# Performance work log

Measured on AMD Instinct MI355X. Metric: run time of the kernel, lower is better.

Reference implementation:

```python
import jax, jax.numpy as jnp
import numpy as np

T = 2048          # num tokens (single prefill sequence)
H = 32            # num local heads
HIDDEN = 5120
Q_LORA = 1536
KV_LORA = 512
D_NOPE = 128
D_ROPE = 64
D_QK = D_NOPE + D_ROPE   # 192
D_V = 128
EPS = 1e-6
SCALING = D_QK ** -0.5


def _rope_tables(theta=10000.0):
    inv_freq = 1.0 / (theta ** (np.arange(0, D_ROPE, 2, dtype=np.float32) / D_ROPE))
    t = np.arange(T, dtype=np.float32)
    freqs = np.outer(t, inv_freq)                       # [T, D_ROPE/2]
    emb = np.concatenate([freqs, freqs], axis=-1)       # [T, D_ROPE]
    return (jnp.asarray(np.cos(emb))[:, None, :],       # [T,1,D_ROPE]
            jnp.asarray(np.sin(emb))[:, None, :])


def setup_inputs() -> dict:
    key = jax.random.key(0)
    ks = jax.random.split(key, 6)
    cos, sin = _rope_tables()
    s = lambda fan_in: 1.0 / np.sqrt(fan_in)
    return {
        'hidden_states': jax.random.normal(ks[0], (T, HIDDEN), jnp.float32),
        'cos': cos,
        'sin': sin,
        'wq_a': jax.random.normal(ks[1], (HIDDEN, Q_LORA), jnp.float32) * s(HIDDEN),
        'q_a_ln_w': jnp.ones((Q_LORA,), jnp.float32),
        'wq_b': jax.random.normal(ks[2], (Q_LORA, H * D_QK), jnp.float32) * s(Q_LORA),
        'wkv_a': jax.random.normal(ks[3], (HIDDEN, KV_LORA + D_ROPE), jnp.float32) * s(HIDDEN),
        'kv_a_ln_w': jnp.ones((KV_LORA,), jnp.float32),
        'wkv_b': jax.random.normal(ks[4], (KV_LORA, H * (D_NOPE + D_V)), jnp.float32) * s(KV_LORA),
        'wo': jax.random.normal(ks[5], (H * D_V, HIDDEN), jnp.float32) * s(H * D_V),
    }


def _rmsnorm(x, w):
    var = jnp.mean(jnp.square(x), axis=-1, keepdims=True)
    return x * jax.lax.rsqrt(var + EPS) * w


def _deinterleave(x):
    # torch: x.view(..., d//2, 2).transpose(-1,-2).reshape(..., d)
    return jnp.concatenate([x[..., 0::2], x[..., 1::2]], axis=-1)


def _rotate_half(x):
    h = x.shape[-1] // 2
    return jnp.concatenate([-x[..., h:], x[..., :h]], axis=-1)


def _apply_rope(q, k, cos, sin):
    q = _deinterleave(q)
    k = _deinterleave(k)
    return q * cos + _rotate_half(q) * sin, k * cos + _rotate_half(k) * sin


def reference(hidden_states, cos, sin, wq_a, q_a_ln_w, wq_b, wkv_a, kv_a_ln_w, wkv_b, wo):
    # Q path: low-rank down-proj, RMSNorm, up-proj
    q = _rmsnorm(hidden_states @ wq_a, q_a_ln_w) @ wq_b
    q = q.reshape(T, H, D_QK)
    q_nope, q_pe = q[..., :D_NOPE], q[..., D_NOPE:]

    # KV path: joint compressed latent + rope key slice
    ckv = hidden_states @ wkv_a
    compressed, k_pe = ckv[..., :KV_LORA], ckv[..., KV_LORA:].reshape(T, 1, D_ROPE)
    kv = (_rmsnorm(compressed, kv_a_ln_w) @ wkv_b).reshape(T, H, D_NOPE + D_V)
    k_nope, value = kv[..., :D_NOPE], kv[..., D_NOPE:]

    # split RoPE on the rope sub-dims only
    q_pe, k_pe = _apply_rope(q_pe, k_pe, cos, sin)
    q = jnp.concatenate([q_nope, q_pe], axis=-1)                    # [T,H,192]
    k = jnp.concatenate([k_nope, jnp.broadcast_to(k_pe, (T, H, D_ROPE))], axis=-1)

    # causal attention (prefill)
    scores = jnp.einsum('qhd,khd->hqk', q, k) * SCALING             # [H,T,T]
    mask = jnp.tril(jnp.ones((T, T), bool))
    scores = jnp.where(mask[None], scores, jnp.finfo(scores.dtype).min)
    probs = jax.nn.softmax(scores, axis=-1)
    attn = jnp.einsum('hqk,khd->qhd', probs, value)                 # [T,H,128]

    return attn.reshape(T, H * D_V) @ wo                            # [T,HIDDEN]
```

## Files before the change

kernel.cpp:

```cpp
#include <hip/hip_runtime.h>
#include <hip/hip_bf16.h>
#include <stdint.h>

typedef __hip_bfloat16 bf16;
typedef short v8s __attribute__((ext_vector_type(8)));
typedef float v4f __attribute__((ext_vector_type(4)));

#define T_SEQ 2048
#define NH 32
#define HIDDEN_D 5120
#define QL 1536
#define KVL 512
#define DQK 192
#define DV 128
#define NAB 2176
#define SCALE_QK 0.07216878364870322f

static __device__ __forceinline__ float b2f(bf16 x) { return __bfloat162float(x); }
static __device__ __forceinline__ bf16 f2b(float x) { return __float2bfloat16(x); }
static __device__ __forceinline__ unsigned short bbits(bf16 x) {
  union { bf16 b; unsigned short u; } c; c.b = x; return c.u;
}

#define AS1(p) ((__attribute__((address_space(1))) void*)(p))
#define AS3(p) ((__attribute__((address_space(3))) void*)(p))

__global__ void detect_k(const void* __restrict__ lnw, int* __restrict__ flag) {
  if (threadIdx.x == 0 && blockIdx.x == 0) {
    uint32_t u = *(const uint32_t*)lnw;
    flag[0] = ((u & 0xFFFFu) == 0x3F80u) ? 1 : 0;
  }
}

__global__ __launch_bounds__(256) void conv_bf16(const void* __restrict__ in,
        bf16* __restrict__ out, const int* __restrict__ flag, int n4) {
  int i = blockIdx.x * 256 + threadIdx.x;
  if (i >= n4) return;
  if (flag[0]) {
    ((uint2*)out)[i] = ((const uint2*)in)[i];
  } else {
    float4 v = ((const float4*)in)[i];
    uint2 o;
    o.x = ((uint32_t)bbits(f2b(v.y)) << 16) | bbits(f2b(v.x));
    o.y = ((uint32_t)bbits(f2b(v.w)) << 16) | bbits(f2b(v.z));
    ((uint2*)out)[i] = o;
  }
}

__global__ __launch_bounds__(256) void transpose_any(const void* __restrict__ in,
        bf16* __restrict__ out, int R, int C, int Cpad, const int* __restrict__ flag) {
  __shared__ unsigned short tile[32][33];
  const int isb = flag[0];
  int c0 = blockIdx.x * 32, r0 = blockIdx.y * 32;
  int tx = threadIdx.x, ty = threadIdx.y;
#pragma unroll
  for (int i = 0; i < 32; i += 8) {
    unsigned short v = 0;
    int c = c0 + tx;
    if (c < C) {
      size_t idx = (size_t)(r0 + ty + i) * C + c;
      v = isb ? *((const unsigned short*)in + idx)
              : bbits(f2b(((const float*)in)[idx]));
    }
    tile[ty + i][tx] = v;
  }
  __syncthreads();
#pragma unroll
  for (int i = 0; i < 32; i += 8) {
    int c = c0 + ty + i;
    if (c < Cpad) *(unsigned short*)&out[(size_t)c * R + r0 + tx] = tile[tx][ty + i];
  }
}

template <bool FINAL>
__global__ __launch_bounds__(256, 2)
void gemm_bt(const bf16* __restrict__ A, const bf16* __restrict__ Bt,
             void* __restrict__ C, const int* __restrict__ flag,
             int M, int N, int K) {
  __shared__ __align__(16) bf16 As[128 * 32];
  __shared__ __align__(16) bf16 Bs[128 * 32];
  const int tid = threadIdx.x;
  const int wv = tid >> 6;
  const int lane = tid & 63;
  const int quad = lane >> 4;
  const int c16 = lane & 15;
  const int wm = (wv & 1) * 64;
  const int wn = (wv >> 1) * 64;
  const int m0 = blockIdx.y * 128;
  const int n0 = blockIdx.x * 128;

  v4f acc[4][4] = {};

  const int r0 = tid >> 2;
  const int cc0 = (tid & 3) << 3;

  for (int k0 = 0; k0 < K; k0 += 32) {
    __syncthreads();
#pragma unroll
    for (int i = 0; i < 2; ++i) {
      int r = r0 + i * 64;
      const bf16* ga = A + (size_t)(m0 + r) * K + k0 + cc0;
      const bf16* gb = Bt + (size_t)(n0 + r) * K + k0 + cc0;
      __builtin_amdgcn_global_load_lds(AS1(ga), AS3(As + (i * 256 + wv * 64) * 8), 16, 0, 0);
      __builtin_amdgcn_global_load_lds(AS1(gb), AS3(Bs + (i * 256 + wv * 64) * 8), 16, 0, 0);
    }
    __syncthreads();
    v8s af[4], bfr[4];
#pragma unroll
    for (int t = 0; t < 4; ++t)
      af[t] = *(const v8s*)(As + (wm + t * 16 + c16) * 32 + quad * 8);
#pragma unroll
    for (int t = 0; t < 4; ++t)
      bfr[t] = *(const v8s*)(Bs + (wn + t * 16 + c16) * 32 + quad * 8);
#pragma unroll
    for (int i = 0; i < 4; ++i)
#pragma unroll
      for (int j = 0; j < 4; ++j)
        acc[i][j] = __builtin_amdgcn_mfma_f32_16x16x32_bf16(af[i], bfr[j], acc[i][j], 0, 0, 0);
  }
  const bool outBf = FINAL ? (flag[0] != 0) : true;
#pragma unroll
  for (int i = 0; i < 4; ++i)
#pragma unroll
    for (int j = 0; j < 4; ++j) {
      int m = m0 + wm + i * 16 + quad * 4;
      int n = n0 + wn + j * 16 + c16;
#pragma unroll
      for (int r = 0; r < 4; ++r) {
        if (outBf) ((bf16*)C)[(size_t)(m + r) * N + n] = f2b(acc[i][j][r]);
        else       ((float*)C)[(size_t)(m + r) * N + n] = acc[i][j][r];
      }
    }
}

template <int N>
__global__ __launch_bounds__(256) void rmsnorm_k(const bf16* __restrict__ in,
        const void* __restrict__ w, const int* __restrict__ flag,
        bf16* __restrict__ out, int strideIn, int strideOut) {
  constexpr int CNT = N / 256;
  const int row = blockIdx.x, tid = threadIdx.x;
  const int isb = flag[0];
  const bf16* x = in + (size_t)row * strideIn;
  float v[CNT];
  float ss = 0.f;
#pragma unroll
  for (int i = 0; i < CNT; ++i) { v[i] = b2f(x[tid + i * 256]); ss += v[i] * v[i]; }
#pragma unroll
  for (int o = 32; o > 0; o >>= 1) ss += __shfl_xor(ss, o);
  __shared__ float wsum[4];
  if ((tid & 63) == 0) wsum[tid >> 6] = ss;
  __syncthreads();
  float scale = rsqrtf((wsum[0] + wsum[1] + wsum[2] + wsum[3]) / (float)N + 1e-6f);
#pragma unroll
  for (int i = 0; i < CNT; ++i) {
    int c = tid + i * 256;
    float wv = isb ? b2f(((const bf16*)w)[c]) : ((const float*)w)[c];
    out[(size_t)row * strideOut + c] = f2b(v[i] * scale * wv);
  }
}

__global__ __launch_bounds__(256) void qk_build(const bf16* __restrict__ qraw,
        const bf16* __restrict__ ckv, const bf16* __restrict__ kv,
        const void* __restrict__ cosb, const void* __restrict__ sinb,
        const int* __restrict__ flag,
        bf16* __restrict__ Qh, bf16* __restrict__ Kh) {
  const int t = blockIdx.x, tid = threadIdx.x;
  const int isb = flag[0];
  __shared__ float cs[64], sn[64], kpe[64];
  if (tid < 64) {
    int j = tid;
    float c = isb ? b2f(((const bf16*)cosb)[t * 64 + j]) : ((const float*)cosb)[t * 64 + j];
    float s = isb ? b2f(((const bf16*)sinb)[t * 64 + j]) : ((const float*)sinb)[t * 64 + j];
    cs[j] = c; sn[j] = s;
    const bf16* kp = ckv + (size_t)t * NAB + 512;
    float v;
    if (j < 32) v = b2f(kp[2 * j]) * c - b2f(kp[2 * j + 1]) * s;
    else { int i2 = j - 32; v = b2f(kp[2 * i2 + 1]) * c + b2f(kp[2 * i2]) * s; }
    kpe[j] = v;
  }
  __syncthreads();
  for (int idx = tid; idx < 512; idx += 256) {
    int h = idx >> 4, d8 = (idx & 15) * 8;
    *(uint4*)&Qh[((size_t)h * T_SEQ + t) * DQK + d8] =
        *(const uint4*)&qraw[(size_t)t * 6144 + h * DQK + d8];
    *(uint4*)&Kh[((size_t)h * T_SEQ + t) * DQK + d8] =
        *(const uint4*)&kv[(size_t)t * 8192 + h * 256 + d8];
  }
  for (int idx = tid; idx < 2048; idx += 256) {
    int h = idx >> 6, j = idx & 63;
    const bf16* qp = qraw + (size_t)t * 6144 + h * DQK + 128;
    float v;
    if (j < 32) v = b2f(qp[2 * j]) * cs[j] - b2f(qp[2 * j + 1]) * sn[j];
    else { int i2 = j - 32; v = b2f(qp[2 * i2 + 1]) * cs[j] + b2f(qp[2 * i2]) * sn[j]; }
    Qh[((size_t)h * T_SEQ + t) * DQK + 128 + j] = f2b(v);
    Kh[((size_t)h * T_SEQ + t) * DQK + 128 + j] = f2b(kpe[j]);
  }
}

__global__ __launch_bounds__(256) void vt_build(const bf16* __restrict__ kv,
                                                bf16* __restrict__ VT) {
  __shared__ unsigned short tile[32][33];
  int h = blockIdx.z;
  int t0 = blockIdx.x * 32, d0 = blockIdx.y * 32;
  int tx = threadIdx.x, ty = threadIdx.y;
#pragma unroll
  for (int i = 0; i < 32; i += 8)
    tile[ty + i][tx] = *(const unsigned short*)
        &kv[(size_t)(t0 + ty + i) * 8192 + h * 256 + 128 + d0 + tx];
  __syncthreads();
#pragma unroll
  for (int i = 0; i < 32; i += 8)
    *(unsigned short*)&VT[((size_t)h * DV + d0 + ty + i) * T_SEQ + t0 + tx] = tile[tx][ty + i];
}

__global__ __launch_bounds__(256, 2)
void mla_attn(const bf16* __restrict__ Qh, const bf16* __restrict__ Kh,
              const bf16* __restrict__ VT, bf16* __restrict__ attn) {
  const int wg = blockIdx.x + blockIdx.y * 16;
  const int swz = (wg & 7) * 64 + (wg >> 3);
  const int pid = swz & 15, h = swz >> 4;
  const int tid = threadIdx.x, wv = tid >> 6, lane = tid & 63;
  const int quad = lane >> 4, c16 = lane & 15;

  __shared__ __align__(16) bf16 Ksh[64 * 200];
  __shared__ __align__(16) bf16 Vsh[128 * 72];
  __shared__ __align__(16) bf16 Psh[4 * 16 * 72];
  bf16* pw = Psh + wv * (16 * 72);

#pragma unroll 1
  for (int pass = 0; pass < 2; ++pass) {
    const int qt = (pass == 0) ? pid : (31 - pid);
    const int qbase = qt * 64;

    v8s qf[6];
    {
      const bf16* qp = Qh + ((size_t)h * T_SEQ + qbase + wv * 16 + c16) * DQK;
#pragma unroll
      for (int ks = 0; ks < 6; ++ks) qf[ks] = *(const v8s*)(qp + ks * 32 + quad * 8);
    }

    v4f oacc[8] = {};
    float mrow[4] = {-1e30f, -1e30f, -1e30f, -1e30f};
    float lrow[4] = {0.f, 0.f, 0.f, 0.f};

    for (int kt = 0; kt <= qt; ++kt) {
      const int kb = kt * 64;
      __syncthreads();
      for (int c = tid; c < 1536; c += 256) {
        int r = c / 24, off = (c % 24) * 8;
        *(uint4*)(Ksh + r * 200 + off) =
            *(const uint4*)(Kh + ((size_t)h * T_SEQ + kb + r) * DQK + off);
      }
      for (int c = tid; c < 1024; c += 256) {
        int r = c >> 3, off = (c & 7) * 8;
        *(uint4*)(Vsh + r * 72 + off) =
            *(const uint4*)(VT + ((size_t)h * DV + r) * T_SEQ + kb + off);
      }
      __syncthreads();

      v4f sacc[4] = {};
#pragma unroll
      for (int nt = 0; nt < 4; ++nt)
#pragma unroll
        for (int ks = 0; ks < 6; ++ks) {
          v8s kf = *(const v8s*)(Ksh + (nt * 16 + c16) * 200 + ks * 32 + quad * 8);
          sacc[nt] = __builtin_amdgcn_mfma_f32_16x16x32_bf16(qf[ks], kf, sacc[nt], 0, 0, 0);
        }

      float rmax[4] = {-1e30f, -1e30f, -1e30f, -1e30f};
      const int rowg = qbase + wv * 16 + quad * 4;
#pragma unroll
      for (int nt = 0; nt < 4; ++nt) {
        int col = kb + nt * 16 + c16;
#pragma unroll
        for (int r = 0; r < 4; ++r) {
          float s = sacc[nt][r] * SCALE_QK;
          if (col > rowg + r) s = -1e30f;
          sacc[nt][r] = s;
          rmax[r] = fmaxf(rmax[r], s);
        }
      }
#pragma unroll
      for (int r = 0; r < 4; ++r)
#pragma unroll
        for (int o = 8; o > 0; o >>= 1) rmax[r] = fmaxf(rmax[r], __shfl_xor(rmax[r], o));

      float alpha[4], rsum[4];
#pragma unroll
      for (int r = 0; r < 4; ++r) {
        float mnew = fmaxf(mrow[r], rmax[r]);
        alpha[r] = __expf(mrow[r] - mnew);
        mrow[r] = mnew;
        rsum[r] = 0.f;
      }
#pragma unroll
      for (int nt = 0; nt < 4; ++nt)
#pragma unroll
        for (int r = 0; r < 4; ++r) {
          float p = __expf(sacc[nt][r] - mrow[r]);
          sacc[nt][r] = p;
          rsum[r] += p;
        }
#pragma unroll
      for (int r = 0; r < 4; ++r) {
#pragma unroll
        for (int o = 8; o > 0; o >>= 1) rsum[r] += __shfl_xor(rsum[r], o);
        lrow[r] = lrow[r] * alpha[r] + rsum[r];
      }
#pragma unroll
      for (int i = 0; i < 8; ++i)
#pragma unroll
        for (int r = 0; r < 4; ++r) oacc[i][r] *= alpha[r];

#pragma unroll
      for (int nt = 0; nt < 4; ++nt)
#pragma unroll
        for (int r = 0; r < 4; ++r)
          pw[(quad * 4 + r) * 72 + nt * 16 + c16] = f2b(sacc[nt][r]);

#pragma unroll
      for (int ks = 0; ks < 2; ++ks) {
        v8s paf = *(const v8s*)(pw + c16 * 72 + ks * 32 + quad * 8);
#pragma unroll
        for (int nt = 0; nt < 8; ++nt) {
          v8s vf = *(const v8s*)(Vsh + (nt * 16 + c16) * 72 + ks * 32 + quad * 8);
          oacc[nt] = __builtin_amdgcn_mfma_f32_16x16x32_bf16(paf, vf, oacc[nt], 0, 0, 0);
        }
      }
    }

#pragma unroll
    for (int r = 0; r < 4; ++r) {
      float inv = 1.f / lrow[r];
      int trow = qbase + wv * 16 + quad * 4 + r;
#pragma unroll
      for (int nt = 0; nt < 8; ++nt)
        attn[(size_t)trow * 4096 + h * DV + nt * 16 + c16] = f2b(oacc[nt][r] * inv);
    }
  }
}

extern "C" void kernel_launch(void* const* d_in, const int* in_sizes, int n_in,
                              void* d_out, int out_size, void* d_ws, size_t ws_size,
                              hipStream_t stream) {
  (void)in_sizes; (void)n_in; (void)out_size; (void)ws_size;
  const void* hidden   = d_in[0];
  const void* cosb     = d_in[1];
  const void* sinb     = d_in[2];
  const void* wq_a     = d_in[3];
  const void* q_a_ln_w = d_in[4];
  const void* wq_b     = d_in[5];
  const void* wkv_a    = d_in[6];
  const void* kv_a_ln_w= d_in[7];
  const void* wkv_b    = d_in[8];
  const void* wo       = d_in[9];

  int* flag = (int*)d_ws;
  bf16* ws  = (bf16*)d_ws + 16;

  size_t o = 0;
  bf16* wqaT  = ws + o; o += (size_t)QL * HIDDEN_D;
  bf16* wkvaT = ws + o; o += (size_t)640 * HIDDEN_D;
  bf16* wqbT  = ws + o; o += (size_t)6144 * QL;
  bf16* wkvbT = ws + o; o += (size_t)8192 * KVL;
  bf16* woT   = ws + o; o += (size_t)HIDDEN_D * 4096;
  bf16* Hb    = ws + o; o += (size_t)T_SEQ * HIDDEN_D;
  bf16* Cab   = ws + o; o += (size_t)T_SEQ * NAB;
  bf16* q_raw = ws + o; o += (size_t)T_SEQ * 6144;
  bf16* attn  = q_raw;
  bf16* kv    = ws + o; o += (size_t)T_SEQ * 8192;
  bf16* Qh    = ws + o; o += (size_t)NH * T_SEQ * DQK;
  bf16* Kh    = ws + o; o += (size_t)NH * T_SEQ * DQK;
  bf16* VT    = ws + o; o += (size_t)NH * DV * T_SEQ;
  bf16* q_a_n = Qh;
  bf16* ckv_n = Qh + (size_t)T_SEQ * QL;

  detect_k<<<1, 64, 0, stream>>>(q_a_ln_w, flag);

  conv_bf16<<<(T_SEQ * HIDDEN_D / 4 + 255) / 256, 256, 0, stream>>>(hidden, Hb, flag,
                                                                    T_SEQ * HIDDEN_D / 4);
  dim3 b32(32, 8);
  transpose_any<<<dim3(1536/32, 5120/32), b32, 0, stream>>>(wq_a,  wqaT, 5120, 1536, 1536, flag);
  transpose_any<<<dim3(6144/32, 1536/32), b32, 0, stream>>>(wq_b,  wqbT, 1536, 6144, 6144, flag);
  transpose_any<<<dim3(640/32,  5120/32), b32, 0, stream>>>(wkv_a, wkvaT, 5120, 576, 640, flag);
  transpose_any<<<dim3(8192/32, 512/32),  b32, 0, stream>>>(wkv_b, wkvbT, 512, 8192, 8192, flag);
  transpose_any<<<dim3(5120/32, 4096/32), b32, 0, stream>>>(wo,    woT, 4096, 5120, 5120, flag);

  gemm_bt<false><<<dim3(NAB/128, 16), 256, 0, stream>>>(Hb, wqaT, Cab, flag, T_SEQ, NAB, HIDDEN_D);
  rmsnorm_k<1536><<<T_SEQ, 256, 0, stream>>>(Cab, q_a_ln_w, flag, q_a_n, NAB, 1536);
  gemm_bt<false><<<dim3(6144/128, 16), 256, 0, stream>>>(q_a_n, wqbT, q_raw, flag, T_SEQ, 6144, 1536);
  rmsnorm_k<512><<<T_SEQ, 256, 0, stream>>>(Cab + QL, kv_a_ln_w, flag, ckv_n, NAB, 512);
  gemm_bt<false><<<dim3(8192/128, 16), 256, 0, stream>>>(ckv_n, wkvbT, kv, flag, T_SEQ, 8192, 512);

  qk_build<<<T_SEQ, 256, 0, stream>>>(q_raw, Cab + QL, kv, cosb, sinb, flag, Qh, Kh);
  vt_build<<<dim3(T_SEQ/32, DV/32, NH), b32, 0, stream>>>(kv, VT);
  mla_attn<<<dim3(16, NH), 256, 0, stream>>>(Qh, Kh, VT, attn);

  gemm_bt<true><<<dim3(5120/128, 16), 256, 0, stream>>>(attn, woT, d_out, flag, T_SEQ, 5120, 4096);
}
```

Baseline: 906.3 us.

## Add 256x256-tile pipelined bf16 GEMM for q_b, kv_b and output projections

Introduces a new GEMM kernel with 256x256 output tiles, 512 threads and a 4-slot shared-memory ring. Tiles are filled by direct global-to-LDS loads, with explicit vmcnt waits and raised wave priority around the MFMA loop. It replaces the 128-tile GEMM for the q up-projection, the kv up-projection and the output projection, aiming for more data reuse per block and better overlap of loads with compute. The larger tiles cut the number of blocks (160–256) on a device with many compute units, which can leave CUs idle. The 128 KB of shared memory limits occupancy to one block per CU.

```diff
diff --git a/kernel.cpp b/kernel.cpp
--- a/kernel.cpp
+++ b/kernel.cpp
@@ -125,6 +125,87 @@
     for (int j = 0; j < 4; ++j) {
       int m = m0 + wm + i * 16 + quad * 4;
       int n = n0 + wn + j * 16 + c16;
+#pragma unroll
+      for (int r = 0; r < 4; ++r) {
+        if (outBf) ((bf16*)C)[(size_t)(m + r) * N + n] = f2b(acc[i][j][r]);
+        else       ((float*)C)[(size_t)(m + r) * N + n] = acc[i][j][r];
+      }
+    }
+}
+
+template <bool FINAL>
+__global__ __launch_bounds__(512, 2)
+void gemm_bt256(const bf16* __restrict__ A, const bf16* __restrict__ Bt,
+                void* __restrict__ C, const int* __restrict__ flag,
+                int M, int N, int K) {
+  __shared__ __align__(16) bf16 sA[4][256 * 32];
+  __shared__ __align__(16) bf16 sB[4][256 * 32];
+  const int tid = threadIdx.x;
+  const int wv = tid >> 6, lane = tid & 63;
+  const int quad = lane >> 4, c16 = lane & 15;
+  const int wr = wv >> 2, wc = wv & 3;
+  const int m0 = blockIdx.y * 256, n0 = blockIdx.x * 256;
+  const int NT = K >> 5;
+
+  const int srow = tid >> 2, scol = (tid & 3) << 3;
+
+  auto stage = [&](int t) {
+    const int k0 = t << 5, slot = t & 3;
+#pragma unroll
+    for (int r = 0; r < 2; ++r) {
+      int c = r * 512 + tid;
+      __builtin_amdgcn_global_load_lds(
+          AS1(A + (size_t)(m0 + srow + r * 128) * K + k0 + scol),
+          AS3(&sA[slot][c * 8]), 16, 0, 0);
+    }
+#pragma unroll
+    for (int r = 0; r < 2; ++r) {
+      int c = r * 512 + tid;
+      __builtin_amdgcn_global_load_lds(
+          AS1(Bt + (size_t)(n0 + srow + r * 128) * K + k0 + scol),
+          AS3(&sB[slot][c * 8]), 16, 0, 0);
+    }
+  };
+
+  v4f acc[8][4] = {};
+
+  stage(0);
+  if (NT > 1) stage(1);
+  if (NT > 2) stage(2);
+
+  for (int t = 0; t < NT; ++t) {
+    if (t + 2 < NT)      { asm volatile("s_waitcnt vmcnt(8)" ::: "memory"); }
+    else if (t + 1 < NT) { asm volatile("s_waitcnt vmcnt(4)" ::: "memory"); }
+    else                 { asm volatile("s_waitcnt vmcnt(0)" ::: "memory"); }
+    __builtin_amdgcn_sched_barrier(0);
+    __builtin_amdgcn_s_barrier();
+    __builtin_amdgcn_sched_barrier(0);
+    if (t + 3 < NT) stage(t + 3);
+
+    const bf16* As = sA[t & 3];
+    const bf16* Bs = sB[t & 3];
+    v8s bfr[4];
+#pragma unroll
+    for (int j = 0; j < 4; ++j)
+      bfr[j] = *(const v8s*)(Bs + (wc * 64 + j * 16 + c16) * 32 + quad * 8);
+    __builtin_amdgcn_s_setprio(1);
+#pragma unroll
+    for (int i = 0; i < 8; ++i) {
+      v8s af = *(const v8s*)(As + (wr * 128 + i * 16 + c16) * 32 + quad * 8);
+#pragma unroll
+      for (int j = 0; j < 4; ++j)
+        acc[i][j] = __builtin_amdgcn_mfma_f32_16x16x32_bf16(af, bfr[j], acc[i][j], 0, 0, 0);
+    }
+    __builtin_amdgcn_s_setprio(0);
+  }
+
+  const bool outBf = FINAL ? (flag[0] != 0) : true;
+#pragma unroll
+  for (int i = 0; i < 8; ++i)
+#pragma unroll
+    for (int j = 0; j < 4; ++j) {
+      int m = m0 + wr * 128 + i * 16 + quad * 4;
+      int n = n0 + wc * 64 + j * 16 + c16;
 #pragma unroll
       for (int r = 0; r < 4; ++r) {
         if (outBf) ((bf16*)C)[(size_t)(m + r) * N + n] = f2b(acc[i][j][r]);
@@ -388,13 +469,16 @@
 
   gemm_bt<false><<<dim3(NAB/128, 16), 256, 0, stream>>>(Hb, wqaT, Cab, flag, T_SEQ, NAB, HIDDEN_D);
   rmsnorm_k<1536><<<T_SEQ, 256, 0, stream>>>(Cab, q_a_ln_w, flag, q_a_n, NAB, 1536);
-  gemm_bt<false><<<dim3(6144/128, 16), 256, 0, stream>>>(q_a_n, wqbT, q_raw, flag, T_SEQ, 6144, 1536);
+  gemm_bt256<false><<<dim3(6144/256, 2048/256), 512, 0, stream>>>(q_a_n, wqbT, q_raw, flag,
+                                                                  T_SEQ, 6144, 1536);
   rmsnorm_k<512><<<T_SEQ, 256, 0, stream>>>(Cab + QL, kv_a_ln_w, flag, ckv_n, NAB, 512);
-  gemm_bt<false><<<dim3(8192/128, 16), 256, 0, stream>>>(ckv_n, wkvbT, kv, flag, T_SEQ, 8192, 512);
+  gemm_bt256<false><<<dim3(8192/256, 2048/256), 512, 0, stream>>>(ckv_n, wkvbT, kv, flag,
+                                                                  T_SEQ, 8192, 512);
 
   qk_build<<<T_SEQ, 256, 0, stream>>>(q_raw, Cab + QL, kv, cosb, sinb, flag, Qh, Kh);
   vt_build<<<dim3(T_SEQ/32, DV/32, NH), b32, 0, stream>>>(kv, VT);
   mla_attn<<<dim3(16, NH), 256, 0, stream>>>(Qh, Kh, VT, attn);
 
-  gemm_bt<true><<<dim3(5120/128, 16), 256, 0, stream>>>(attn, woT, d_out, flag, T_SEQ, 5120, 4096);
-}
+  gemm_bt256<true><<<dim3(5120/256, 2048/256), 512, 0, stream>>>(attn, woT, d_out, flag,
+                                                                 T_SEQ, 5120, 4096);
+}
```

After: 943.7 us. 1.04x slower.
